# Performance work log

Measured on AMD Instinct MI355X. Metric: run time of the kernel, lower is better.

The kernel has to match this reference:

```python
import jax, jax.numpy as jnp
import numpy as np

N, D, K = 131072, 256, 16      # samples, ambient dim, projection dims
NDOM, B, G = 8, 32, 100        # domains, hist_bins, barycenter grid size


def setup_inputs() -> dict:
    key = jax.random.key(0)
    k1, k2, k3, k4, k5, k6 = jax.random.split(key, 6)
    X = jax.random.normal(k1, (N, D), jnp.float32)
    y = jax.random.randint(k2, (N,), 0, NDOM)
    # wT: orthonormal columns via QR with sign fix (as in INB.__init__)
    wi = np.asarray(jax.random.normal(k3, (D, K), jnp.float32))
    Q, R = np.linalg.qr(wi)
    wT = jnp.asarray(Q * np.sign(np.diag(R)), jnp.float32)
    # Per-(domain, dim) histogram bin edges (sorted -> monotone) and CDF values in [0,1]
    bin_edges = jnp.sort(jax.random.normal(k4, (NDOM, K, B + 1), jnp.float32) * 2.0, axis=-1)
    steps = jax.random.uniform(k5, (NDOM, K, B), jnp.float32, minval=0.1, maxval=1.0)
    c = jnp.cumsum(steps, axis=-1)
    cdf_vals = jnp.concatenate([jnp.zeros((NDOM, K, 1), jnp.float32), c / c[..., -1:]], axis=-1)
    # Barycenter inverse-CDF (quantile function) sampled on a uniform grid over [0,1]
    bary_q = jnp.sort(jax.random.normal(k6, (K, G), jnp.float32) * 2.0, axis=-1)
    return {"X": X, "y": y, "wT": wT, "bin_edges": bin_edges,
            "cdf_vals": cdf_vals, "bary_q": bary_q}


def _searchsorted_2d(edges, x):
    # edges: (N, K, B+1) per-sample monotone edges; x: (N, K)
    ss = jax.vmap(jax.vmap(lambda e, v: jnp.searchsorted(e, v, side='right')))(edges, x)
    return jnp.clip(ss - 1, 0, B - 1)  # (N, K) int, left bin index


def reference(X, y, wT, bin_edges, cdf_vals, bary_q):
    Xm = X @ wT                         # (N, K) small-K GEMM
    remaining = X - Xm @ wT.T           # (N, D)
    # gather per-sample domain tables (irregular, data-dependent access)
    eb = bin_edges[y]                   # (N, K, B+1)
    cb = cdf_vals[y]                    # (N, K, B+1)
    i = _searchsorted_2d(eb, Xm)        # (N, K)
    x0 = jnp.take_along_axis(eb, i[..., None], axis=-1)[..., 0]
    x1 = jnp.take_along_axis(eb, i[..., None] + 1, axis=-1)[..., 0]
    f0 = jnp.take_along_axis(cb, i[..., None], axis=-1)[..., 0]
    f1 = jnp.take_along_axis(cb, i[..., None] + 1, axis=-1)[..., 0]
    t = jnp.clip((Xm - x0) / (x1 - x0), 0.0, 1.0)
    u = f0 + t * (f1 - f0)              # per-domain CDF value in [0,1]
    # barycenter inverse CDF: linear interp on uniform grid over [0,1]
    pos = jnp.clip(u, 0.0, 1.0) * (G - 1)
    j = jnp.clip(pos.astype(jnp.int32), 0, G - 2)
    tt = pos - j.astype(pos.dtype)
    kk = jnp.arange(K)[None, :]
    z = bary_q[kk, j] * (1.0 - tt) + bary_q[kk, j + 1] * tt  # (N, K)
    return remaining + z @ wT.T
```

## Files before the change

kernel.cpp:

```cpp
#include <hip/hip_runtime.h>

typedef float v2f __attribute__((ext_vector_type(2)));
typedef float v4f __attribute__((ext_vector_type(4)));

#define N_ROWS 131072
#define DIM    256
#define KP     16
#define NDOM   8
#define NB     32
#define GG     100

#define EB_N   (NDOM*KP*(NB+1))
#define BARY_N (KP*GG)

#define GRID   1024
#define WAVES  4
#define NWAVE  (GRID*WAVES)
#define PAIRS  16

__device__ __forceinline__ void pl32swap(float &a, float &b) {
    asm("v_permlane32_swap_b32 %0, %1" : "+v"(a), "+v"(b));
}
__device__ __forceinline__ void pl16swap(float &a, float &b) {
    asm("v_permlane16_swap_b32 %0, %1" : "+v"(a), "+v"(b));
}
__device__ __forceinline__ v2f swap32_sum(v2f lo, v2f hi) {
    float a0 = lo[0], b0 = hi[0], a1 = lo[1], b1 = hi[1];
    pl32swap(a0, b0); pl32swap(a1, b1);
    v2f r; r[0] = a0 + b0; r[1] = a1 + b1; return r;
}
__device__ __forceinline__ v2f swap16_sum(v2f lo, v2f hi) {
    float a0 = lo[0], b0 = hi[0], a1 = lo[1], b1 = hi[1];
    pl16swap(a0, b0); pl16swap(a1, b1);
    v2f r; r[0] = a0 + b0; r[1] = a1 + b1; return r;
}
template <int CTRL>
__device__ __forceinline__ float dppf(float x) {
    return __builtin_bit_cast(float, __builtin_amdgcn_update_dpp(
        0, __builtin_bit_cast(int, x), CTRL, 0xF, 0xF, true));
}
template <int CTRL>
__device__ __forceinline__ int dppi(int x) {
    return __builtin_amdgcn_update_dpp(0, x, CTRL, 0xF, 0xF, true);
}
__device__ __forceinline__ float red16(float v) {
    v += dppf<0xB1>(v);
    v += dppf<0x4E>(v);
    v += dppf<0x141>(v);
    v += dppf<0x140>(v);
    return v;
}
__device__ __forceinline__ void wave_fence() {
    asm volatile("s_waitcnt lgkmcnt(0)" ::: "memory");
    __builtin_amdgcn_sched_barrier(0);
}

__device__ __forceinline__ float reduce_scatter(v2f P[8], int lane) {
    v2f Q[4];
#pragma unroll
    for (int r = 0; r < 4; ++r)
        Q[r] = swap32_sum(P[r], P[r+4]);
    v2f S0 = swap16_sum(Q[0], Q[2]);
    v2f S1 = swap16_sum(Q[1], Q[3]);
    float a = red16(S0[0]), b = red16(S0[1]);
    float c = red16(S1[0]), d = red16(S1[1]);
    float lo = (lane & 1) ? b : a;
    float hi = (lane & 1) ? d : c;
    return (lane & 2) ? hi : lo;
}

__device__ __forceinline__ float quantile_map(float xm, const float* ebRow,
                                              const float* cfRow, const float* bqk,
                                              const float e[8]) {
    int cnt = (e[0] <= xm) + (e[1] <= xm) + (e[2] <= xm) + (e[3] <= xm)
            + (e[4] <= xm) + (e[5] <= xm) + (e[6] <= xm) + (e[7] <= xm);
    cnt += dppi<0x124>(cnt);
    cnt += dppi<0x128>(cnt);
    int i0 = min(max(cnt - 1, 0), NB - 1);
    float x0 = ebRow[i0], x1 = ebRow[i0+1];
    float f0 = cfRow[i0], f1 = cfRow[i0+1];
    float t  = fminf(fmaxf(__fdividef(xm - x0, x1 - x0), 0.f), 1.f);
    float u  = f0 + t * (f1 - f0);
    float posv = fminf(fmaxf(u, 0.f), 1.f) * (float)(GG - 1);
    int jj = min((int)posv, GG - 2);
    float ttf = posv - (float)jj;
    float b0 = bqk[jj], b1 = bqk[jj+1];
    return xm - (b0*(1.f - ttf) + b1*ttf);
}

__device__ __forceinline__ void proj_row(v4f x, const v2f wTo[4][8], v2f P[8]) {
#pragma unroll
    for (int q = 0; q < 8; ++q) P[q] = (v2f){0.f, 0.f};
#pragma unroll
    for (int j = 0; j < 4; ++j) {
        v2f xj = {x[j], x[j]};
#pragma unroll
        for (int q = 0; q < 8; ++q) P[q] += xj * wTo[j][q];
    }
}

__device__ __forceinline__ void out_row(v4f x, const float* cb, const v2f wTo[4][8],
                                        float* op) {
    v2f c2[8];
#pragma unroll
    for (int q = 0; q < 4; ++q) {
        v4f cv4 = *reinterpret_cast<const v4f*>(&cb[4*q]);
        c2[2*q]   = (v2f){cv4[0], cv4[1]};
        c2[2*q+1] = (v2f){cv4[2], cv4[3]};
    }
    v4f o4;
#pragma unroll
    for (int j = 0; j < 4; ++j) {
        v2f a = c2[0] * wTo[j][0];
#pragma unroll
        for (int q = 1; q < 8; ++q) a += c2[q] * wTo[j][q];
        o4[j] = x[j] - (a[0] + a[1]);
    }
    *reinterpret_cast<v4f*>(op) = o4;
}

__global__ __launch_bounds__(256, 4)
void inb_kernel(const float* __restrict__ X, const int* __restrict__ y,
                const float* __restrict__ wT, const float* __restrict__ be,
                const float* __restrict__ cv, const float* __restrict__ bq,
                float* __restrict__ out)
{
    __shared__ alignas(16) float sEB[EB_N];
    __shared__ alignas(16) float sCDF[EB_N];
    __shared__ alignas(16) float sBARY[BARY_N];
    __shared__ alignas(16) float sCOEFF[WAVES][32];

    const int tid = threadIdx.x;
    for (int i = tid; i < EB_N; i += 256) { sEB[i] = be[i]; sCDF[i] = cv[i]; }
    for (int i = tid; i < BARY_N; i += 256) sBARY[i] = bq[i];
    __syncthreads();

    const int lane = tid & 63;
    const int wid  = tid >> 6;
    const int k  = ((lane & 48) >> 2) | (lane & 3);
    const int ec = (lane >> 2) & 3;

    v2f wTo[4][8];
#pragma unroll
    for (int j = 0; j < 4; ++j) {
        const v4f* wrow = reinterpret_cast<const v4f*>(&wT[(4*lane + j)*KP]);
#pragma unroll
        for (int q = 0; q < 4; ++q) {
            v4f v = wrow[q];
            wTo[j][2*q]   = (v2f){v[0], v[1]};
            wTo[j][2*q+1] = (v2f){v[2], v[3]};
        }
    }

    float* cobuf = sCOEFF[wid];
    const int gwave = blockIdx.x * WAVES + wid;
    const int xoff  = 4*lane;

    v4f xA = *reinterpret_cast<const v4f*>(&X[(size_t)gwave*DIM + xoff]);
    v4f xB = *reinterpret_cast<const v4f*>(&X[(size_t)(gwave + NWAVE)*DIM + xoff]);
    int dA = y[gwave], dB = y[gwave + NWAVE];

    for (int it = 0; it < PAIRS; ++it) {
        const int rA = gwave + (2*it)*NWAVE;
        const int rB = rA + NWAVE;

        const float* ebA = &sEB[(dA*KP + k)*(NB+1)];
        const float* ebB = &sEB[(dB*KP + k)*(NB+1)];
        float eA[8], eB[8];
#pragma unroll
        for (int t = 0; t < 8; ++t) { eA[t] = ebA[8*ec + t]; eB[t] = ebB[8*ec + t]; }

        int nA = rA + 2*NWAVE; if (nA >= N_ROWS) nA = rA;
        int nB = nA + NWAVE;   if (nB >= N_ROWS) nB = rA;
        int dA_n = y[nA], dB_n = y[nB];
        v4f xA_n = *reinterpret_cast<const v4f*>(&X[(size_t)nA*DIM + xoff]);
        v4f xB_n = *reinterpret_cast<const v4f*>(&X[(size_t)nB*DIM + xoff]);

        v2f PA[8], PB[8];
        proj_row(xA, wTo, PA);
        proj_row(xB, wTo, PB);

        float xmA = reduce_scatter(PA, lane);
        float xmB = reduce_scatter(PB, lane);

        float cA = quantile_map(xmA, ebA, &sCDF[(dA*KP + k)*(NB+1)], &sBARY[k*GG], eA);
        float cB = quantile_map(xmB, ebB, &sCDF[(dB*KP + k)*(NB+1)], &sBARY[k*GG], eB);

        if (ec < 2) cobuf[ec*16 + k] = (ec == 0) ? cA : cB;
        wave_fence();

        out_row(xA, cobuf,      wTo, &out[(size_t)rA*DIM + xoff]);
        out_row(xB, cobuf + 16, wTo, &out[(size_t)rB*DIM + xoff]);

        xA = xA_n; xB = xB_n; dA = dA_n; dB = dB_n;
    }
}

extern "C" void kernel_launch(void* const* d_in, const int* in_sizes, int n_in,
                              void* d_out, int out_size, void* d_ws, size_t ws_size,
                              hipStream_t stream) {
    const float* X  = (const float*)d_in[0];
    const int*   y  = (const int*)  d_in[1];
    const float* wT = (const float*)d_in[2];
    const float* be = (const float*)d_in[3];
    const float* cv = (const float*)d_in[4];
    const float* bq = (const float*)d_in[5];
    float* out = (float*)d_out;
    hipLaunchKernelGGL(inb_kernel, dim3(GRID), dim3(256), 0, stream,
                       X, y, wT, be, cv, bq, out);
}
```

Measured before the change: 69.23 us.

## Process four rows per iteration and replace permlane swaps with shuffles

The per-wave loop now handles four rows per iteration instead of two, prefetching the next four X rows and domain labels so more loads are in flight. The cross-half reductions now use __shfl_xor (ds_bpermute) instead of inline v_permlane32/16_swap asm. The goal is more memory-level parallelism in a bandwidth-bound kernel. In exchange, register pressure rises under the 4-blocks-per-SM launch bound, which risks spills, and the shuffle path may cost more than the native permlane swaps.

```diff
diff --git a/kernel.cpp b/kernel.cpp
--- a/kernel.cpp
+++ b/kernel.cpp
@@ -16,23 +16,25 @@
 #define GRID   1024
 #define WAVES  4
 #define NWAVE  (GRID*WAVES)
-#define PAIRS  16
-
-__device__ __forceinline__ void pl32swap(float &a, float &b) {
-    asm("v_permlane32_swap_b32 %0, %1" : "+v"(a), "+v"(b));
-}
-__device__ __forceinline__ void pl16swap(float &a, float &b) {
-    asm("v_permlane16_swap_b32 %0, %1" : "+v"(a), "+v"(b));
-}
-__device__ __forceinline__ v2f swap32_sum(v2f lo, v2f hi) {
-    float a0 = lo[0], b0 = hi[0], a1 = lo[1], b1 = hi[1];
-    pl32swap(a0, b0); pl32swap(a1, b1);
-    v2f r; r[0] = a0 + b0; r[1] = a1 + b1; return r;
-}
-__device__ __forceinline__ v2f swap16_sum(v2f lo, v2f hi) {
-    float a0 = lo[0], b0 = hi[0], a1 = lo[1], b1 = hi[1];
-    pl16swap(a0, b0); pl16swap(a1, b1);
-    v2f r; r[0] = a0 + b0; r[1] = a1 + b1; return r;
+#define QUADS  8
+
+__device__ __forceinline__ v2f swap32_sum(v2f lo, v2f hi, int lane) {
+    bool up = (lane & 32) != 0;
+    v2f keep = up ? hi : lo;
+    v2f send = up ? lo : hi;
+    v2f r;
+    r[0] = keep[0] + __shfl_xor(send[0], 32);
+    r[1] = keep[1] + __shfl_xor(send[1], 32);
+    return r;
+}
+__device__ __forceinline__ v2f swap16_sum(v2f lo, v2f hi, int lane) {
+    bool up = (lane & 16) != 0;
+    v2f keep = up ? hi : lo;
+    v2f send = up ? lo : hi;
+    v2f r;
+    r[0] = keep[0] + __shfl_xor(send[0], 16);
+    r[1] = keep[1] + __shfl_xor(send[1], 16);
+    return r;
 }
 template <int CTRL>
 __device__ __forceinline__ float dppf(float x) {
@@ -55,13 +57,24 @@
     __builtin_amdgcn_sched_barrier(0);
 }
 
+__device__ __forceinline__ void proj_row(v4f x, const v2f wTo[4][8], v2f P[8]) {
+#pragma unroll
+    for (int q = 0; q < 8; ++q) P[q] = (v2f){0.f, 0.f};
+#pragma unroll
+    for (int j = 0; j < 4; ++j) {
+        v2f xj = {x[j], x[j]};
+#pragma unroll
+        for (int q = 0; q < 8; ++q) P[q] += xj * wTo[j][q];
+    }
+}
+
 __device__ __forceinline__ float reduce_scatter(v2f P[8], int lane) {
     v2f Q[4];
 #pragma unroll
     for (int r = 0; r < 4; ++r)
-        Q[r] = swap32_sum(P[r], P[r+4]);
-    v2f S0 = swap16_sum(Q[0], Q[2]);
-    v2f S1 = swap16_sum(Q[1], Q[3]);
+        Q[r] = swap32_sum(P[r], P[r+4], lane);
+    v2f S0 = swap16_sum(Q[0], Q[2], lane);
+    v2f S1 = swap16_sum(Q[1], Q[3], lane);
     float a = red16(S0[0]), b = red16(S0[1]);
     float c = red16(S1[0]), d = red16(S1[1]);
     float lo = (lane & 1) ? b : a;
@@ -88,17 +101,6 @@
     return xm - (b0*(1.f - ttf) + b1*ttf);
 }
 
-__device__ __forceinline__ void proj_row(v4f x, const v2f wTo[4][8], v2f P[8]) {
-#pragma unroll
-    for (int q = 0; q < 8; ++q) P[q] = (v2f){0.f, 0.f};
-#pragma unroll
-    for (int j = 0; j < 4; ++j) {
-        v2f xj = {x[j], x[j]};
-#pragma unroll
-        for (int q = 0; q < 8; ++q) P[q] += xj * wTo[j][q];
-    }
-}
-
 __device__ __forceinline__ void out_row(v4f x, const float* cb, const v2f wTo[4][8],
                                         float* op) {
     v2f c2[8];
@@ -153,46 +155,74 @@
     }
 
     float* cobuf = sCOEFF[wid];
+    const float* bqk = &sBARY[k*GG];
     const int gwave = blockIdx.x * WAVES + wid;
     const int xoff  = 4*lane;
 
-    v4f xA = *reinterpret_cast<const v4f*>(&X[(size_t)gwave*DIM + xoff]);
-    v4f xB = *reinterpret_cast<const v4f*>(&X[(size_t)(gwave + NWAVE)*DIM + xoff]);
-    int dA = y[gwave], dB = y[gwave + NWAVE];
-
-    for (int it = 0; it < PAIRS; ++it) {
-        const int rA = gwave + (2*it)*NWAVE;
-        const int rB = rA + NWAVE;
+    v4f xA = *reinterpret_cast<const v4f*>(&X[(size_t)(gwave          )*DIM + xoff]);
+    v4f xB = *reinterpret_cast<const v4f*>(&X[(size_t)(gwave +   NWAVE)*DIM + xoff]);
+    v4f xC = *reinterpret_cast<const v4f*>(&X[(size_t)(gwave + 2*NWAVE)*DIM + xoff]);
+    v4f xD = *reinterpret_cast<const v4f*>(&X[(size_t)(gwave + 3*NWAVE)*DIM + xoff]);
+    int dA = y[gwave], dB = y[gwave + NWAVE], dC = y[gwave + 2*NWAVE], dD = y[gwave + 3*NWAVE];
+
+    for (int it = 0; it < QUADS; ++it) {
+        const int rA = gwave + (4*it)*NWAVE;
+        const int rB = rA + NWAVE, rC = rA + 2*NWAVE, rD = rA + 3*NWAVE;
 
         const float* ebA = &sEB[(dA*KP + k)*(NB+1)];
         const float* ebB = &sEB[(dB*KP + k)*(NB+1)];
-        float eA[8], eB[8];
-#pragma unroll
-        for (int t = 0; t < 8; ++t) { eA[t] = ebA[8*ec + t]; eB[t] = ebB[8*ec + t]; }
-
-        int nA = rA + 2*NWAVE; if (nA >= N_ROWS) nA = rA;
+        const float* ebC = &sEB[(dC*KP + k)*(NB+1)];
+        const float* ebD = &sEB[(dD*KP + k)*(NB+1)];
+        float eA[8], eB[8], eC[8], eD[8];
+#pragma unroll
+        for (int t = 0; t < 8; ++t) {
+            eA[t] = ebA[8*ec + t]; eB[t] = ebB[8*ec + t];
+            eC[t] = ebC[8*ec + t]; eD[t] = ebD[8*ec + t];
+        }
+
+        int nA = rA + 4*NWAVE; if (nA >= N_ROWS) nA = rA;
         int nB = nA + NWAVE;   if (nB >= N_ROWS) nB = rA;
-        int dA_n = y[nA], dB_n = y[nB];
+        int nC = nA + 2*NWAVE; if (nC >= N_ROWS) nC = rA;
+        int nD = nA + 3*NWAVE; if (nD >= N_ROWS) nD = rA;
+        int dA_n = y[nA], dB_n = y[nB], dC_n = y[nC], dD_n = y[nD];
         v4f xA_n = *reinterpret_cast<const v4f*>(&X[(size_t)nA*DIM + xoff]);
         v4f xB_n = *reinterpret_cast<const v4f*>(&X[(size_t)nB*DIM + xoff]);
-
-        v2f PA[8], PB[8];
-        proj_row(xA, wTo, PA);
-        proj_row(xB, wTo, PB);
-
-        float xmA = reduce_scatter(PA, lane);
-        float xmB = reduce_scatter(PB, lane);
-
-        float cA = quantile_map(xmA, ebA, &sCDF[(dA*KP + k)*(NB+1)], &sBARY[k*GG], eA);
-        float cB = quantile_map(xmB, ebB, &sCDF[(dB*KP + k)*(NB+1)], &sBARY[k*GG], eB);
+        v4f xC_n = *reinterpret_cast<const v4f*>(&X[(size_t)nC*DIM + xoff]);
+        v4f xD_n = *reinterpret_cast<const v4f*>(&X[(size_t)nD*DIM + xoff]);
+
+        float xmA, xmB, xmC, xmD;
+        {
+            v2f PA[8], PB[8];
+            proj_row(xA, wTo, PA);
+            proj_row(xB, wTo, PB);
+            xmA = reduce_scatter(PA, lane);
+            xmB = reduce_scatter(PB, lane);
+        }
+        {
+            v2f PC[8], PD[8];
+            proj_row(xC, wTo, PC);
+            proj_row(xD, wTo, PD);
+            xmC = reduce_scatter(PC, lane);
+            xmD = reduce_scatter(PD, lane);
+        }
+
+        float cA = quantile_map(xmA, ebA, &sCDF[(dA*KP + k)*(NB+1)], bqk, eA);
+        float cB = quantile_map(xmB, ebB, &sCDF[(dB*KP + k)*(NB+1)], bqk, eB);
+        float cC = quantile_map(xmC, ebC, &sCDF[(dC*KP + k)*(NB+1)], bqk, eC);
+        float cD = quantile_map(xmD, ebD, &sCDF[(dD*KP + k)*(NB+1)], bqk, eD);
 
         if (ec < 2) cobuf[ec*16 + k] = (ec == 0) ? cA : cB;
         wave_fence();
-
         out_row(xA, cobuf,      wTo, &out[(size_t)rA*DIM + xoff]);
         out_row(xB, cobuf + 16, wTo, &out[(size_t)rB*DIM + xoff]);
 
-        xA = xA_n; xB = xB_n; dA = dA_n; dB = dB_n;
+        if (ec < 2) cobuf[ec*16 + k] = (ec == 0) ? cC : cD;
+        wave_fence();
+        out_row(xC, cobuf,      wTo, &out[(size_t)rC*DIM + xoff]);
+        out_row(xD, cobuf + 16, wTo, &out[(size_t)rD*DIM + xoff]);
+
+        xA = xA_n; xB = xB_n; xC = xC_n; xD = xD_n;
+        dA = dA_n; dB = dB_n; dC = dC_n; dD = dD_n;
     }
 }
 
```

After: 176.1 us. 2.54x slower.

## Read CDF and barycenter tables from global memory, double grid, use shuffles

Applied to the files above, without the earlier changes.

Drops the shared-memory copies of the CDF and barycenter tables and reads them straight from global memory, which should hit in cache, so each block does less setup staging and uses less LDS. The grid doubles while each wave handles half as many row pairs, which raises block count and cuts per-block serial work. The permlane swap reductions are replaced with __shfl_xor exchanges plus selects. The risks are added global-load latency in the quantile map and shuffles that may be slower than permlane swaps.

```diff
diff --git a/kernel.cpp b/kernel.cpp
--- a/kernel.cpp
+++ b/kernel.cpp
@@ -13,26 +13,28 @@
 #define EB_N   (NDOM*KP*(NB+1))
 #define BARY_N (KP*GG)
 
-#define GRID   1024
+#define GRID   2048
 #define WAVES  4
 #define NWAVE  (GRID*WAVES)
-#define PAIRS  16
-
-__device__ __forceinline__ void pl32swap(float &a, float &b) {
-    asm("v_permlane32_swap_b32 %0, %1" : "+v"(a), "+v"(b));
-}
-__device__ __forceinline__ void pl16swap(float &a, float &b) {
-    asm("v_permlane16_swap_b32 %0, %1" : "+v"(a), "+v"(b));
-}
-__device__ __forceinline__ v2f swap32_sum(v2f lo, v2f hi) {
-    float a0 = lo[0], b0 = hi[0], a1 = lo[1], b1 = hi[1];
-    pl32swap(a0, b0); pl32swap(a1, b1);
-    v2f r; r[0] = a0 + b0; r[1] = a1 + b1; return r;
-}
-__device__ __forceinline__ v2f swap16_sum(v2f lo, v2f hi) {
-    float a0 = lo[0], b0 = hi[0], a1 = lo[1], b1 = hi[1];
-    pl16swap(a0, b0); pl16swap(a1, b1);
-    v2f r; r[0] = a0 + b0; r[1] = a1 + b1; return r;
+#define PAIRS  8
+
+__device__ __forceinline__ v2f swap32_sum(v2f lo, v2f hi, int lane) {
+    bool up = (lane & 32) != 0;
+    v2f keep = up ? hi : lo;
+    v2f send = up ? lo : hi;
+    v2f r;
+    r[0] = keep[0] + __shfl_xor(send[0], 32);
+    r[1] = keep[1] + __shfl_xor(send[1], 32);
+    return r;
+}
+__device__ __forceinline__ v2f swap16_sum(v2f lo, v2f hi, int lane) {
+    bool up = (lane & 16) != 0;
+    v2f keep = up ? hi : lo;
+    v2f send = up ? lo : hi;
+    v2f r;
+    r[0] = keep[0] + __shfl_xor(send[0], 16);
+    r[1] = keep[1] + __shfl_xor(send[1], 16);
+    return r;
 }
 template <int CTRL>
 __device__ __forceinline__ float dppf(float x) {
@@ -55,13 +57,24 @@
     __builtin_amdgcn_sched_barrier(0);
 }
 
+__device__ __forceinline__ void proj_row(v4f x, const v2f wTo[4][8], v2f P[8]) {
+#pragma unroll
+    for (int q = 0; q < 8; ++q) P[q] = (v2f){0.f, 0.f};
+#pragma unroll
+    for (int j = 0; j < 4; ++j) {
+        v2f xj = {x[j], x[j]};
+#pragma unroll
+        for (int q = 0; q < 8; ++q) P[q] += xj * wTo[j][q];
+    }
+}
+
 __device__ __forceinline__ float reduce_scatter(v2f P[8], int lane) {
     v2f Q[4];
 #pragma unroll
     for (int r = 0; r < 4; ++r)
-        Q[r] = swap32_sum(P[r], P[r+4]);
-    v2f S0 = swap16_sum(Q[0], Q[2]);
-    v2f S1 = swap16_sum(Q[1], Q[3]);
+        Q[r] = swap32_sum(P[r], P[r+4], lane);
+    v2f S0 = swap16_sum(Q[0], Q[2], lane);
+    v2f S1 = swap16_sum(Q[1], Q[3], lane);
     float a = red16(S0[0]), b = red16(S0[1]);
     float c = red16(S1[0]), d = red16(S1[1]);
     float lo = (lane & 1) ? b : a;
@@ -88,17 +101,6 @@
     return xm - (b0*(1.f - ttf) + b1*ttf);
 }
 
-__device__ __forceinline__ void proj_row(v4f x, const v2f wTo[4][8], v2f P[8]) {
-#pragma unroll
-    for (int q = 0; q < 8; ++q) P[q] = (v2f){0.f, 0.f};
-#pragma unroll
-    for (int j = 0; j < 4; ++j) {
-        v2f xj = {x[j], x[j]};
-#pragma unroll
-        for (int q = 0; q < 8; ++q) P[q] += xj * wTo[j][q];
-    }
-}
-
 __device__ __forceinline__ void out_row(v4f x, const float* cb, const v2f wTo[4][8],
                                         float* op) {
     v2f c2[8];
@@ -126,13 +128,10 @@
                 float* __restrict__ out)
 {
     __shared__ alignas(16) float sEB[EB_N];
-    __shared__ alignas(16) float sCDF[EB_N];
-    __shared__ alignas(16) float sBARY[BARY_N];
     __shared__ alignas(16) float sCOEFF[WAVES][32];
 
     const int tid = threadIdx.x;
-    for (int i = tid; i < EB_N; i += 256) { sEB[i] = be[i]; sCDF[i] = cv[i]; }
-    for (int i = tid; i < BARY_N; i += 256) sBARY[i] = bq[i];
+    for (int i = tid; i < EB_N; i += 256) sEB[i] = be[i];
     __syncthreads();
 
     const int lane = tid & 63;
@@ -153,6 +152,7 @@
     }
 
     float* cobuf = sCOEFF[wid];
+    const float* bqk = bq + k*GG;
     const int gwave = blockIdx.x * WAVES + wid;
     const int xoff  = 4*lane;
 
@@ -183,8 +183,8 @@
         float xmA = reduce_scatter(PA, lane);
         float xmB = reduce_scatter(PB, lane);
 
-        float cA = quantile_map(xmA, ebA, &sCDF[(dA*KP + k)*(NB+1)], &sBARY[k*GG], eA);
-        float cB = quantile_map(xmB, ebB, &sCDF[(dB*KP + k)*(NB+1)], &sBARY[k*GG], eB);
+        float cA = quantile_map(xmA, ebA, cv + (size_t)(dA*KP + k)*(NB+1), bqk, eA);
+        float cB = quantile_map(xmB, ebB, cv + (size_t)(dB*KP + k)*(NB+1), bqk, eB);
 
         if (ec < 2) cobuf[ec*16 + k] = (ec == 0) ? cA : cB;
         wave_fence();
```

Result: slower. 77.50 us (+12.0%).
